# Performance work log

Measured on AMD Instinct MI355X. Metric: run time of the kernel, lower is better.

## Reference

```python
import jax, jax.numpy as jnp
from jax import lax
import numpy as np

# pywt sym4 analysis filters (pywt.Wavelet('sym4').dec_lo / .dec_hi)
DEC_LO = np.array([-0.07576571478927333, -0.02963552764599851, 0.49761866763201545,
                   0.8037387518059161, 0.29785779560527736, -0.09921954357684722,
                   -0.012603967262037833, 0.0322231006040427], dtype=np.float32)
DEC_HI = np.array([-0.0322231006040427, -0.012603967262037833, 0.09921954357684722,
                   0.29785779560527736, -0.8037387518059161, 0.49761866763201545,
                   0.02963552764599851, -0.07576571478927333], dtype=np.float32)
L = 8            # sym4 filter length
LEVEL = 4
THRESH = 10.0


def _conv1d(x, kernel, stride, pad):
    # x: (B, T), kernel: (L,) used in correlation sense by lax.conv
    y = lax.conv_general_dilated(x[:, None, :], kernel[None, None, :],
                                 window_strides=(stride,), padding=[pad],
                                 dimension_numbers=('NCH', 'OIH', 'NCH'))
    return y[:, 0, :]


def _dwt1(x, filt):
    # pywt single-level DWT, mode='symmetric':
    #   pad L-1 each side (half-sample symmetric), true convolution, take odd-index
    #   outputs of the 'valid' part -> length floor((N+L-1)/2)
    ext = jnp.pad(x, ((0, 0), (L - 1, L - 1)), mode='symmetric')[:, 1:]
    return _conv1d(ext, filt[::-1], 2, (0, 0))  # flip -> true convolution


def _idwt1(cA, cD, lo, hi):
    # pywt single-level IDWT: upsample by 2, full-convolve with rec filters, sum,
    # trim L-2 from the left, output length 2*n - L + 2.
    B, n = cA.shape
    upA = jnp.zeros((B, 2 * n), cA.dtype).at[:, ::2].set(cA)
    upD = jnp.zeros((B, 2 * n), cD.dtype).at[:, ::2].set(cD)
    # rec_lo = dec_lo[::-1]; full conv w/ rec_lo == correlation w/ dec_lo
    y = _conv1d(upA, lo, 1, (L - 1, L - 1)) + _conv1d(upD, hi, 1, (L - 1, L - 1))
    return y[:, L - 2: L - 2 + 2 * n - L + 2]


def _wavelet_denoise(x):
    lo = jnp.asarray(DEC_LO)
    hi = jnp.asarray(DEC_HI)
    a = x
    details = []
    for _ in range(LEVEL):
        details.append(_dwt1(a, hi))
        a = _dwt1(a, lo)
    # hard threshold: KEEP coefficients with |c| <= threshold, zero the rest
    details = [jnp.where(jnp.abs(d) <= THRESH, d, jnp.zeros_like(d)) for d in details]
    rec = a
    for d in reversed(details):
        if rec.shape[1] > d.shape[1]:     # pywt waverec a[:-1] trim
            rec = rec[:, :d.shape[1]]
        rec = _idwt1(rec, d, lo, hi)
    return rec


def setup_inputs() -> dict:
    key = jax.random.key(0)
    k1, k2 = jax.random.split(key)
    x = jax.random.normal(k1, (100000, 512), dtype=jnp.float32) * 20.0
    edge_index = jax.random.randint(k2, (2, 100000), 0, 100000, dtype=jnp.int64)
    return {"x": x, "edge_index": edge_index, "num_nodes": 100000}


def reference(x, edge_index, num_nodes):
    # edge_index / num_nodes are unused by the original forward
    return _wavelet_denoise(x)
```

## Files before the change

### kernel.cpp

```cpp
#include <hip/hip_runtime.h>
#include <cstddef>

typedef float f2 __attribute__((ext_vector_type(2)));
typedef float f4 __attribute__((ext_vector_type(4)));
typedef _Float16 h2 __attribute__((ext_vector_type(2)));

#define THRESH_V 10.0f
#define WPB 2
#define SLICE_F2 928

static __device__ __forceinline__ void wave_sync() {
  asm volatile("s_waitcnt lgkmcnt(0)" ::: "memory");
}

#define L0f (-0.07576571478927333f)
#define L1f (-0.02963552764599851f)
#define L2f ( 0.49761866763201545f)
#define L3f ( 0.8037387518059161f)
#define L4f ( 0.29785779560527736f)
#define L5f (-0.09921954357684722f)
#define L6f (-0.012603967262037833f)
#define L7f ( 0.0322231006040427f)
#define H0f (-0.0322231006040427f)
#define H1f (-0.012603967262037833f)
#define H2f ( 0.09921954357684722f)
#define H3f ( 0.29785779560527736f)
#define H4f (-0.8037387518059161f)
#define H5f ( 0.49761866763201545f)
#define H6f ( 0.02963552764599851f)
#define H7f (-0.07576571478927333f)

static __device__ __forceinline__ f2 lo2(f4 w) { return __builtin_shufflevector(w, w, 0, 1); }
static __device__ __forceinline__ f2 hi2(f4 w) { return __builtin_shufflevector(w, w, 2, 3); }

template <int N, bool MARGINS, bool D16>
static __device__ __forceinline__ void fwd_stage(const f2* __restrict__ in,
                                                 f2* __restrict__ ca,
                                                 void* __restrict__ cdv, int lane) {
#pragma clang fp contract(off)
  constexpr int M = (N + 7) >> 1;
  f2* const cdf = (f2*)cdv;
  h2* const cdh = (h2*)cdv;
#pragma unroll
  for (int k = 0; k * 64 < M; ++k) {
    const int i = lane + k * 64;
    if (i < M) {
      const f4* w = (const f4*)(in + 2 * i - 6);
      const f4 w0 = w[0], w1 = w[1], w2 = w[2], w3 = w[3];
      const f2 v0 = lo2(w0), v1 = hi2(w0), v2 = lo2(w1), v3 = hi2(w1);
      const f2 v4 = lo2(w2), v5 = hi2(w2), v6 = lo2(w3), v7 = hi2(w3);
      f2 sLo = ((v0 * L7f + v1 * L6f) + (v2 * L5f + v3 * L4f)) +
               ((v4 * L3f + v5 * L2f) + (v6 * L1f + v7 * L0f));
      f2 sHi = ((v0 * H7f + v1 * H6f) + (v2 * H5f + v3 * H4f)) +
               ((v4 * H3f + v5 * H2f) + (v6 * H1f + v7 * H0f));
      ca[i] = sLo;
      if constexpr (MARGINS) {
        if (i < 6)      ca[-1 - i]        = sLo;
        if (i >= M - 7) ca[2 * M - 1 - i] = sLo;
      }
      const float dx = (fabsf(sHi.x) <= THRESH_V) ? sHi.x : 0.f;
      const float dy = (fabsf(sHi.y) <= THRESH_V) ? sHi.y : 0.f;
      if constexpr (D16) {
        h2 r; r.x = (_Float16)dx; r.y = (_Float16)dy;
        cdh[i] = r;
      } else {
        f2 d; d.x = dx; d.y = dy;
        cdf[i] = d;
      }
    }
  }
}

template <int OUTLEN, bool D16, bool GOUT>
static __device__ __forceinline__ void inv_stage(const f2* __restrict__ ca,
                                                 const void* __restrict__ cdv,
                                                 f2* __restrict__ dst,
                                                 float* __restrict__ gA,
                                                 float* __restrict__ gB, bool hasB,
                                                 int lane) {
#pragma clang fp contract(fast)
  const f2* const cf = (const f2*)cdv;
  const h2* const ch = (const h2*)cdv;
  constexpr int PAIRS = (OUTLEN + 1) >> 1;
#pragma unroll
  for (int k = 0; k * 64 < PAIRS; ++k) {
    const int t = lane + k * 64;
    if (t < PAIRS) {
      f2 a0 = ca[t], a1 = ca[t + 1], a2 = ca[t + 2], a3 = ca[t + 3];
      f2 e0, e1, e2, e3;
      if constexpr (D16) {
        h2 x0 = ch[t], x1 = ch[t + 1], x2 = ch[t + 2], x3 = ch[t + 3];
        e0.x = (float)x0.x; e0.y = (float)x0.y;
        e1.x = (float)x1.x; e1.y = (float)x1.y;
        e2.x = (float)x2.x; e2.y = (float)x2.y;
        e3.x = (float)x3.x; e3.y = (float)x3.y;
      } else {
        e0 = cf[t]; e1 = cf[t + 1]; e2 = cf[t + 2]; e3 = cf[t + 3];
      }
      f2 se = a0 * L1f + a1 * L3f + a2 * L5f + a3 * L7f +
              e0 * H1f + e1 * H3f + e2 * H5f + e3 * H7f;
      f2 so = a0 * L0f + a1 * L2f + a2 * L4f + a3 * L6f +
              e0 * H0f + e1 * H2f + e2 * H4f + e3 * H6f;
      const int q = 2 * t;
      if constexpr (GOUT) {
        *reinterpret_cast<float2*>(gA + q) = make_float2(se.x, so.x);
        if (hasB) *reinterpret_cast<float2*>(gB + q) = make_float2(se.y, so.y);
      } else {
        if (q + 1 < OUTLEN) {
          f4 r; r.x = se.x; r.y = se.y; r.z = so.x; r.w = so.y;
          *reinterpret_cast<f4*>(dst + q) = r;
        } else {
          dst[q] = se;
        }
      }
    }
  }
}

__global__ __launch_bounds__(128, 4) void wavelet_denoise_kernel(
    const float* __restrict__ x, float* __restrict__ out, int nrows) {
  __shared__ __align__(16) f2 lds[WPB][SLICE_F2];
  const int wave = threadIdx.x >> 6;
  const int lane = threadIdx.x & 63;
  const int nPairs = (nrows + 1) >> 1;
  const int pairId = blockIdx.x * WPB + wave;
  if (pairId >= nPairs) return;

  const int rA = 2 * pairId;
  const bool hasB = (rA + 1) < nrows;
  const int rBc = hasB ? rA + 1 : rA;

  f2* Sp  = lds[wave];
  f2* sx  = Sp + 6;
  f2* ca2 = Sp + 6;    f2* d2 = Sp + 146;
  f2* ca3 = Sp + 286;  f2* d3 = Sp + 364;
  f2* ca4 = Sp + 434;  f2* d4 = Sp + 472;
  f2* ca1 = Sp + 532;
  h2* d1  = (h2*)(Sp + 798);
  f2* rec70  = Sp + 526;
  f2* rec133 = Sp + 0;
  f2* rec259 = Sp + 526;

  {
    const float4* sA4 = reinterpret_cast<const float4*>(x + (size_t)rA * 512);
    const float4* sB4 = reinterpret_cast<const float4*>(x + (size_t)rBc * 512);
#pragma unroll
    for (int kk = 0; kk < 2; ++kk) {
      const int c = lane + kk * 64;
      const float4 a = sA4[c];
      const float4 b = sB4[c];
      f4 u0; u0.x = a.x; u0.y = b.x; u0.z = a.y; u0.w = b.y;
      f4 u1; u1.x = a.z; u1.y = b.z; u1.z = a.w; u1.w = b.w;
      *reinterpret_cast<f4*>(sx + 4 * c)     = u0;
      *reinterpret_cast<f4*>(sx + 4 * c + 2) = u1;
      if (c == 0) {
        f4 m0; m0.x = a.y; m0.y = b.y; m0.z = a.x; m0.w = b.x;
        *reinterpret_cast<f4*>(sx - 2) = m0;
        f4 m1; m1.x = a.w; m1.y = b.w; m1.z = a.z; m1.w = b.z;
        *reinterpret_cast<f4*>(sx - 4) = m1;
      }
      if (c == 1) {
        f4 m; m.x = a.y; m.y = b.y; m.z = a.x; m.w = b.x;
        *reinterpret_cast<f4*>(sx - 6) = m;
      }
      if (c == 127) {
        f4 m0; m0.x = a.w; m0.y = b.w; m0.z = a.z; m0.w = b.z;
        *reinterpret_cast<f4*>(sx + 512) = m0;
        f4 m1; m1.x = a.y; m1.y = b.y; m1.z = a.x; m1.w = b.x;
        *reinterpret_cast<f4*>(sx + 514) = m1;
      }
      if (c == 126) {
        f4 m0; m0.x = a.w; m0.y = b.w; m0.z = a.z; m0.w = b.z;
        *reinterpret_cast<f4*>(sx + 516) = m0;
        f2 m1; m1.x = a.y; m1.y = b.y;
        sx[518] = m1;
      }
    }
  }
  wave_sync();

  fwd_stage<512, true,  true >(sx,  ca1, d1, lane); wave_sync();
  fwd_stage<259, true,  false>(ca1, ca2, d2, lane); wave_sync();
  fwd_stage<133, true,  false>(ca2, ca3, d3, lane); wave_sync();
  fwd_stage< 70, false, false>(ca3, ca4, d4, lane); wave_sync();

  float* gA = out + (size_t)rA * 512;
  float* gB = out + (size_t)rBc * 512;
  inv_stage< 70, false, false>(ca4,    d4, rec70,  nullptr, nullptr, false, lane);
  wave_sync();
  inv_stage<133, false, false>(rec70,  d3, rec133, nullptr, nullptr, false, lane);
  wave_sync();
  inv_stage<259, false, false>(rec133, d2, rec259, nullptr, nullptr, false, lane);
  wave_sync();
  inv_stage<512, true,  true >(rec259, d1, nullptr, gA, gB, hasB, lane);
}

extern "C" void kernel_launch(void* const* d_in, const int* in_sizes, int n_in,
                              void* d_out, int out_size, void* d_ws, size_t ws_size,
                              hipStream_t stream) {
  const float* x = (const float*)d_in[0];
  float* out = (float*)d_out;
  const int nrows = in_sizes[0] / 512;
  const int nPairs = (nrows + 1) >> 1;
  const int grid = (nPairs + WPB - 1) / WPB;
  wavelet_denoise_kernel<<<dim3(grid), dim3(WPB * 64), 0, stream>>>(x, out, nrows);
}
```

Before: 341.4 us.

## Compute contiguous blocks of outputs per lane to reuse LDS window loads

```diff
diff --git a/kernel.cpp b/kernel.cpp
--- a/kernel.cpp
+++ b/kernel.cpp
@@ -4,10 +4,11 @@
 typedef float f2 __attribute__((ext_vector_type(2)));
 typedef float f4 __attribute__((ext_vector_type(4)));
 typedef _Float16 h2 __attribute__((ext_vector_type(2)));
+typedef _Float16 h8 __attribute__((ext_vector_type(8)));
 
 #define THRESH_V 10.0f
 #define WPB 2
-#define SLICE_F2 928
+#define SLICE_F2 930
 
 static __device__ __forceinline__ void wave_sync() {
   asm volatile("s_waitcnt lgkmcnt(0)" ::: "memory");
@@ -32,8 +33,11 @@
 
 static __device__ __forceinline__ f2 lo2(f4 w) { return __builtin_shufflevector(w, w, 0, 1); }
 static __device__ __forceinline__ f2 hi2(f4 w) { return __builtin_shufflevector(w, w, 2, 3); }
-
-template <int N, bool MARGINS, bool D16>
+static __device__ __forceinline__ float thr(float x) {
+  return (fabsf(x) <= THRESH_V) ? x : 0.f;
+}
+
+template <int N, int B, bool MARGINS, bool D16>
 static __device__ __forceinline__ void fwd_stage(const f2* __restrict__ in,
                                                  f2* __restrict__ ca,
                                                  void* __restrict__ cdv, int lane) {
@@ -41,83 +45,223 @@
   constexpr int M = (N + 7) >> 1;
   f2* const cdf = (f2*)cdv;
   h2* const cdh = (h2*)cdv;
-#pragma unroll
-  for (int k = 0; k * 64 < M; ++k) {
-    const int i = lane + k * 64;
-    if (i < M) {
-      const f4* w = (const f4*)(in + 2 * i - 6);
-      const f4 w0 = w[0], w1 = w[1], w2 = w[2], w3 = w[3];
-      const f2 v0 = lo2(w0), v1 = hi2(w0), v2 = lo2(w1), v3 = hi2(w1);
-      const f2 v4 = lo2(w2), v5 = hi2(w2), v6 = lo2(w3), v7 = hi2(w3);
+  const int i0 = B * lane;
+  if (i0 < M) {
+    f2 w[2 * B + 6];
+    const f4* p = (const f4*)(in + 2 * i0 - 6);
+#pragma unroll
+    for (int k = 0; k < B + 3; ++k) {
+      const f4 t = p[k];
+      w[2 * k] = lo2(t);
+      w[2 * k + 1] = hi2(t);
+    }
+    f2 sA[B], sD[B];
+#pragma unroll
+    for (int j = 0; j < B; ++j) {
+      const f2 v0 = w[2*j+0], v1 = w[2*j+1], v2 = w[2*j+2], v3 = w[2*j+3];
+      const f2 v4 = w[2*j+4], v5 = w[2*j+5], v6 = w[2*j+6], v7 = w[2*j+7];
       f2 sLo = ((v0 * L7f + v1 * L6f) + (v2 * L5f + v3 * L4f)) +
                ((v4 * L3f + v5 * L2f) + (v6 * L1f + v7 * L0f));
       f2 sHi = ((v0 * H7f + v1 * H6f) + (v2 * H5f + v3 * H4f)) +
                ((v4 * H3f + v5 * H2f) + (v6 * H1f + v7 * H0f));
-      ca[i] = sLo;
+      sA[j] = sLo;
+      f2 d; d.x = thr(sHi.x); d.y = thr(sHi.y);
+      sD[j] = d;
       if constexpr (MARGINS) {
-        if (i < 6)      ca[-1 - i]        = sLo;
-        if (i >= M - 7) ca[2 * M - 1 - i] = sLo;
-      }
-      const float dx = (fabsf(sHi.x) <= THRESH_V) ? sHi.x : 0.f;
-      const float dy = (fabsf(sHi.y) <= THRESH_V) ? sHi.y : 0.f;
+        const int i = i0 + j;
+        if (i < 6)                 ca[-1 - i]        = sLo;
+        if (i >= M - 7 && i < M)   ca[2 * M - 1 - i] = sLo;
+      }
+    }
+    if (i0 + B <= M) {
+      if constexpr (B == 4) {
+        f4 c0; c0.x=sA[0].x; c0.y=sA[0].y; c0.z=sA[1].x; c0.w=sA[1].y;
+        f4 c1; c1.x=sA[2].x; c1.y=sA[2].y; c1.z=sA[3].x; c1.w=sA[3].y;
+        *(f4*)(ca + i0)     = c0;
+        *(f4*)(ca + i0 + 2) = c1;
+        if constexpr (D16) {
+          h8 hv;
+          hv[0]=(_Float16)sD[0].x; hv[1]=(_Float16)sD[0].y;
+          hv[2]=(_Float16)sD[1].x; hv[3]=(_Float16)sD[1].y;
+          hv[4]=(_Float16)sD[2].x; hv[5]=(_Float16)sD[2].y;
+          hv[6]=(_Float16)sD[3].x; hv[7]=(_Float16)sD[3].y;
+          *(h8*)(cdh + i0) = hv;
+        } else {
+          f4 d0; d0.x=sD[0].x; d0.y=sD[0].y; d0.z=sD[1].x; d0.w=sD[1].y;
+          f4 d1; d1.x=sD[2].x; d1.y=sD[2].y; d1.z=sD[3].x; d1.w=sD[3].y;
+          *(f4*)(cdf + i0)     = d0;
+          *(f4*)(cdf + i0 + 2) = d1;
+        }
+      } else if constexpr (B == 2) {
+        f4 c0; c0.x=sA[0].x; c0.y=sA[0].y; c0.z=sA[1].x; c0.w=sA[1].y;
+        *(f4*)(ca + i0) = c0;
+        if constexpr (D16) {
+          h2 r0; r0.x=(_Float16)sD[0].x; r0.y=(_Float16)sD[0].y;
+          h2 r1; r1.x=(_Float16)sD[1].x; r1.y=(_Float16)sD[1].y;
+          cdh[i0] = r0; cdh[i0 + 1] = r1;
+        } else {
+          f4 d0; d0.x=sD[0].x; d0.y=sD[0].y; d0.z=sD[1].x; d0.w=sD[1].y;
+          *(f4*)(cdf + i0) = d0;
+        }
+      } else {
+#pragma unroll
+        for (int j = 0; j < B; ++j) {
+          ca[i0 + j] = sA[j];
+          if constexpr (D16) {
+            h2 r; r.x=(_Float16)sD[j].x; r.y=(_Float16)sD[j].y;
+            cdh[i0 + j] = r;
+          } else cdf[i0 + j] = sD[j];
+        }
+      }
+    } else {
+#pragma unroll
+      for (int j = 0; j < B; ++j) {
+        const int i = i0 + j;
+        if (i < M) {
+          ca[i] = sA[j];
+          if constexpr (D16) {
+            h2 r; r.x=(_Float16)sD[j].x; r.y=(_Float16)sD[j].y;
+            cdh[i] = r;
+          } else cdf[i] = sD[j];
+        }
+      }
+    }
+  }
+  if constexpr (64 * B < M) {
+    const int it = 64 * B + lane;
+    if (it < M) {
+      f2 w2[8];
+      const f4* p2 = (const f4*)(in + 2 * it - 6);
+#pragma unroll
+      for (int k = 0; k < 4; ++k) { const f4 t = p2[k]; w2[2*k]=lo2(t); w2[2*k+1]=hi2(t); }
+      const f2 v0=w2[0],v1=w2[1],v2=w2[2],v3=w2[3],v4=w2[4],v5=w2[5],v6=w2[6],v7=w2[7];
+      f2 sLo = ((v0 * L7f + v1 * L6f) + (v2 * L5f + v3 * L4f)) +
+               ((v4 * L3f + v5 * L2f) + (v6 * L1f + v7 * L0f));
+      f2 sHi = ((v0 * H7f + v1 * H6f) + (v2 * H5f + v3 * H4f)) +
+               ((v4 * H3f + v5 * H2f) + (v6 * H1f + v7 * H0f));
+      ca[it] = sLo;
+      if constexpr (MARGINS) {
+        if (it >= M - 7) ca[2 * M - 1 - it] = sLo;
+      }
+      f2 d; d.x = thr(sHi.x); d.y = thr(sHi.y);
       if constexpr (D16) {
-        h2 r; r.x = (_Float16)dx; r.y = (_Float16)dy;
-        cdh[i] = r;
-      } else {
-        f2 d; d.x = dx; d.y = dy;
-        cdf[i] = d;
-      }
-    }
-  }
-}
-
-template <int OUTLEN, bool D16, bool GOUT>
+        h2 r; r.x=(_Float16)d.x; r.y=(_Float16)d.y;
+        cdh[it] = r;
+      } else cdf[it] = d;
+    }
+  }
+}
+
+template <int OUT, int B, bool D16, bool GOUT>
 static __device__ __forceinline__ void inv_stage(const f2* __restrict__ ca,
                                                  const void* __restrict__ cdv,
                                                  f2* __restrict__ dst,
                                                  float* __restrict__ gA,
-                                                 float* __restrict__ gB, bool hasB,
-                                                 int lane) {
+                                                 float* __restrict__ gB,
+                                                 bool hasB, int lane) {
 #pragma clang fp contract(fast)
+  constexpr int P = (OUT + 1) >> 1;
   const f2* const cf = (const f2*)cdv;
   const h2* const ch = (const h2*)cdv;
-  constexpr int PAIRS = (OUTLEN + 1) >> 1;
-#pragma unroll
-  for (int k = 0; k * 64 < PAIRS; ++k) {
-    const int t = lane + k * 64;
-    if (t < PAIRS) {
-      f2 a0 = ca[t], a1 = ca[t + 1], a2 = ca[t + 2], a3 = ca[t + 3];
+  const int t0 = B * lane;
+  if (t0 < P) {
+    f2 a[B + 3], e[B + 3];
+    if constexpr (B == 1) {
+#pragma unroll
+      for (int k = 0; k < 4; ++k) {
+        a[k] = ca[t0 + k];
+        if constexpr (D16) { const h2 hx = ch[t0+k]; e[k].x=(float)hx.x; e[k].y=(float)hx.y; }
+        else e[k] = cf[t0 + k];
+      }
+    } else {
+      constexpr int NR = (B + 4) / 2;
+      const f4* pa = (const f4*)(ca + t0);
+#pragma unroll
+      for (int k = 0; k < NR; ++k) {
+        const f4 t = pa[k];
+        if (2 * k     < B + 3) a[2 * k]     = lo2(t);
+        if (2 * k + 1 < B + 3) a[2 * k + 1] = hi2(t);
+      }
+      if constexpr (D16) {
+        const f4* ph = (const f4*)(ch + t0);
+        const f4 r0 = ph[0], r1 = ph[1];
+        const float rr[8] = {r0.x, r0.y, r0.z, r0.w, r1.x, r1.y, r1.z, r1.w};
+#pragma unroll
+        for (int k = 0; k < B + 3; ++k) {
+          const h2 hx = __builtin_bit_cast(h2, rr[k]);
+          e[k].x = (float)hx.x; e[k].y = (float)hx.y;
+        }
+      } else {
+        const f4* pe = (const f4*)(cf + t0);
+#pragma unroll
+        for (int k = 0; k < NR; ++k) {
+          const f4 t = pe[k];
+          if (2 * k     < B + 3) e[2 * k]     = lo2(t);
+          if (2 * k + 1 < B + 3) e[2 * k + 1] = hi2(t);
+        }
+      }
+    }
+    f2 SE[B], SO[B];
+#pragma unroll
+    for (int j = 0; j < B; ++j) {
+      const f2 a0=a[j], a1=a[j+1], a2=a[j+2], a3=a[j+3];
+      const f2 e0=e[j], e1=e[j+1], e2=e[j+2], e3=e[j+3];
+      SE[j] = a0*L1f + a1*L3f + a2*L5f + a3*L7f +
+              e0*H1f + e1*H3f + e2*H5f + e3*H7f;
+      SO[j] = a0*L0f + a1*L2f + a2*L4f + a3*L6f +
+              e0*H0f + e1*H2f + e2*H4f + e3*H6f;
+    }
+    if constexpr (GOUT) {
+      const int q0 = 2 * t0;
+      *reinterpret_cast<float4*>(gA + q0)     = make_float4(SE[0].x, SO[0].x, SE[1].x, SO[1].x);
+      *reinterpret_cast<float4*>(gA + q0 + 4) = make_float4(SE[2].x, SO[2].x, SE[3].x, SO[3].x);
+      if (hasB) {
+        *reinterpret_cast<float4*>(gB + q0)     = make_float4(SE[0].y, SO[0].y, SE[1].y, SO[1].y);
+        *reinterpret_cast<float4*>(gB + q0 + 4) = make_float4(SE[2].y, SO[2].y, SE[3].y, SO[3].y);
+      }
+    } else {
+      const bool full = (t0 + B <= P) && (2 * (t0 + B) <= OUT);
+      if (full) {
+#pragma unroll
+        for (int j = 0; j < B; ++j) {
+          f4 r; r.x=SE[j].x; r.y=SE[j].y; r.z=SO[j].x; r.w=SO[j].y;
+          *(f4*)(dst + 2 * (t0 + j)) = r;
+        }
+      } else {
+#pragma unroll
+        for (int j = 0; j < B; ++j) {
+          const int t = t0 + j;
+          if (t < P) {
+            const int q = 2 * t;
+            dst[q] = SE[j];
+            if (q + 1 < OUT) dst[q + 1] = SO[j];
+          }
+        }
+      }
+    }
+  }
+  if constexpr (64 * B < P) {
+    const int tt = 64 * B + lane;
+    if (tt < P) {
+      const f2 a0=ca[tt], a1=ca[tt+1], a2=ca[tt+2], a3=ca[tt+3];
       f2 e0, e1, e2, e3;
       if constexpr (D16) {
-        h2 x0 = ch[t], x1 = ch[t + 1], x2 = ch[t + 2], x3 = ch[t + 3];
-        e0.x = (float)x0.x; e0.y = (float)x0.y;
-        e1.x = (float)x1.x; e1.y = (float)x1.y;
-        e2.x = (float)x2.x; e2.y = (float)x2.y;
-        e3.x = (float)x3.x; e3.y = (float)x3.y;
-      } else {
-        e0 = cf[t]; e1 = cf[t + 1]; e2 = cf[t + 2]; e3 = cf[t + 3];
-      }
-      f2 se = a0 * L1f + a1 * L3f + a2 * L5f + a3 * L7f +
-              e0 * H1f + e1 * H3f + e2 * H5f + e3 * H7f;
-      f2 so = a0 * L0f + a1 * L2f + a2 * L4f + a3 * L6f +
-              e0 * H0f + e1 * H2f + e2 * H4f + e3 * H6f;
-      const int q = 2 * t;
-      if constexpr (GOUT) {
-        *reinterpret_cast<float2*>(gA + q) = make_float2(se.x, so.x);
-        if (hasB) *reinterpret_cast<float2*>(gB + q) = make_float2(se.y, so.y);
-      } else {
-        if (q + 1 < OUTLEN) {
-          f4 r; r.x = se.x; r.y = se.y; r.z = so.x; r.w = so.y;
-          *reinterpret_cast<f4*>(dst + q) = r;
-        } else {
-          dst[q] = se;
-        }
-      }
-    }
-  }
-}
-
-__global__ __launch_bounds__(128, 4) void wavelet_denoise_kernel(
+        const h2 x0=ch[tt], x1=ch[tt+1], x2=ch[tt+2], x3=ch[tt+3];
+        e0.x=(float)x0.x; e0.y=(float)x0.y; e1.x=(float)x1.x; e1.y=(float)x1.y;
+        e2.x=(float)x2.x; e2.y=(float)x2.y; e3.x=(float)x3.x; e3.y=(float)x3.y;
+      } else { e0=cf[tt]; e1=cf[tt+1]; e2=cf[tt+2]; e3=cf[tt+3]; }
+      const f2 se = a0*L1f + a1*L3f + a2*L5f + a3*L7f +
+                    e0*H1f + e1*H3f + e2*H5f + e3*H7f;
+      const f2 so = a0*L0f + a1*L2f + a2*L4f + a3*L6f +
+                    e0*H0f + e1*H2f + e2*H4f + e3*H6f;
+      const int q = 2 * tt;
+      dst[q] = se;
+      if (q + 1 < OUT) dst[q + 1] = so;
+    }
+  }
+}
+
+__global__ __launch_bounds__(128, 5) void wavelet_denoise_kernel(
     const float* __restrict__ x, float* __restrict__ out, int nrows) {
   __shared__ __align__(16) f2 lds[WPB][SLICE_F2];
   const int wave = threadIdx.x >> 6;
@@ -134,12 +278,12 @@
   f2* sx  = Sp + 6;
   f2* ca2 = Sp + 6;    f2* d2 = Sp + 146;
   f2* ca3 = Sp + 286;  f2* d3 = Sp + 364;
-  f2* ca4 = Sp + 434;  f2* d4 = Sp + 472;
-  f2* ca1 = Sp + 532;
-  h2* d1  = (h2*)(Sp + 798);
-  f2* rec70  = Sp + 526;
+  f2* ca4 = Sp + 436;  f2* d4 = Sp + 474;
   f2* rec133 = Sp + 0;
-  f2* rec259 = Sp + 526;
+  f2* ca1 = Sp + 530;
+  f2* rec70  = Sp + 524;
+  f2* rec259 = Sp + 524;
+  h2* d1  = (h2*)(Sp + 800);
 
   {
     const float4* sA4 = reinterpret_cast<const float4*>(x + (size_t)rA * 512);
@@ -172,27 +316,25 @@
       if (c == 126) {
         f4 m0; m0.x = a.w; m0.y = b.w; m0.z = a.z; m0.w = b.z;
         *reinterpret_cast<f4*>(sx + 516) = m0;
-        f2 m1; m1.x = a.y; m1.y = b.y;
-        sx[518] = m1;
       }
     }
   }
   wave_sync();
 
-  fwd_stage<512, true,  true >(sx,  ca1, d1, lane); wave_sync();
-  fwd_stage<259, true,  false>(ca1, ca2, d2, lane); wave_sync();
-  fwd_stage<133, true,  false>(ca2, ca3, d3, lane); wave_sync();
-  fwd_stage< 70, false, false>(ca3, ca4, d4, lane); wave_sync();
+  fwd_stage<512, 4, true,  true >(sx,  ca1, d1, lane); wave_sync();
+  fwd_stage<259, 3, true,  false>(ca1, ca2, d2, lane); wave_sync();
+  fwd_stage<133, 2, true,  false>(ca2, ca3, d3, lane); wave_sync();
+  fwd_stage< 70, 1, false, false>(ca3, ca4, d4, lane); wave_sync();
 
   float* gA = out + (size_t)rA * 512;
   float* gB = out + (size_t)rBc * 512;
-  inv_stage< 70, false, false>(ca4,    d4, rec70,  nullptr, nullptr, false, lane);
+  inv_stage< 70, 1, false, false>(ca4,    d4, rec70,  nullptr, nullptr, false, lane);
   wave_sync();
-  inv_stage<133, false, false>(rec70,  d3, rec133, nullptr, nullptr, false, lane);
+  inv_stage<133, 2, false, false>(rec70,  d3, rec133, nullptr, nullptr, false, lane);
   wave_sync();
-  inv_stage<259, false, false>(rec133, d2, rec259, nullptr, nullptr, false, lane);
+  inv_stage<259, 2, false, false>(rec133, d2, rec259, nullptr, nullptr, false, lane);
   wave_sync();
-  inv_stage<512, true,  true >(rec259, d1, nullptr, gA, gB, hasB, lane);
+  inv_stage<512, 4, true,  true >(rec259, d1, nullptr, gA, gB, hasB, lane);
 }
 
 extern "C" void kernel_launch(void* const* d_in, const int* in_sizes, int n_in,
```

Measured after the change: 339.1 us. About the same (-0.7%).
